# Optimization experiments

Hardware: AMD Instinct MI355X
Metric: run time of the kernel (lower is better)

Reference implementation:

```python
import jax, jax.numpy as jnp
import numpy as np

N_NODES = 10000
N_EDGES = 320000
HIDDEN = 64
IN_NODE = 4
IN_EDGE = 2
N_LAYERS = 4
COORDS_WEIGHT = 1.0
EPS = 1e-8


def _linear_params(key, fan_in, fan_out, scale=None, bias=True):
    k1, k2 = jax.random.split(key)
    s = scale if scale is not None else 1.0 / np.sqrt(fan_in)
    w = jax.random.uniform(k1, (fan_in, fan_out), jnp.float32, -s, s)
    b = jax.random.uniform(k2, (fan_out,), jnp.float32, -s, s) if bias else None
    return w, b


def setup_inputs() -> dict:
    key = jax.random.key(0)
    ks = jax.random.split(key, 16)
    his = jax.random.normal(ks[0], (N_NODES, IN_NODE), jnp.float32)
    loc = jax.random.normal(ks[1], (N_NODES, 3), jnp.float32)
    vel = jax.random.normal(ks[2], (N_NODES, 3), jnp.float32)
    edges = jax.random.randint(ks[3], (2, N_EDGES), 0, N_NODES, jnp.int64)
    edge_attr = jax.random.normal(ks[4], (N_EDGES, IN_EDGE), jnp.float32)
    emb_w, emb_b = _linear_params(ks[5], IN_NODE, HIDDEN)
    # edge MLP: cat(h_i, h_j, radial, edge_attr) -> hidden -> hidden
    edge_in = 2 * HIDDEN + 1 + IN_EDGE
    edge_w1, edge_b1 = _linear_params(ks[6], edge_in, HIDDEN)
    edge_w2, edge_b2 = _linear_params(ks[7], HIDDEN, HIDDEN)
    # node MLP: cat(h, agg) -> hidden -> hidden
    node_w1, node_b1 = _linear_params(ks[8], 2 * HIDDEN, HIDDEN)
    node_w2, node_b2 = _linear_params(ks[9], HIDDEN, HIDDEN)
    # coord MLP: hidden -> hidden -> 1 (last layer xavier-small, no bias, as in EGNN)
    coord_w1, coord_b1 = _linear_params(ks[10], HIDDEN, HIDDEN)
    coord_w2 = jax.random.normal(ks[11], (HIDDEN, 1), jnp.float32) * 0.001
    # coord_mlp_vel: hidden -> hidden -> 1
    vel_w1, vel_b1 = _linear_params(ks[12], HIDDEN, HIDDEN)
    vel_w2, vel_b2 = _linear_params(ks[13], HIDDEN, 1)
    return dict(his=his, loc=loc, edges=edges, vel=vel, edge_attr=edge_attr,
                emb_w=emb_w, emb_b=emb_b,
                edge_w1=edge_w1, edge_b1=edge_b1, edge_w2=edge_w2, edge_b2=edge_b2,
                node_w1=node_w1, node_b1=node_b1, node_w2=node_w2, node_b2=node_b2,
                coord_w1=coord_w1, coord_b1=coord_b1, coord_w2=coord_w2,
                vel_w1=vel_w1, vel_b1=vel_b1, vel_w2=vel_w2, vel_b2=vel_b2)


def _segment_mean(data, seg, num_segments):
    s = jax.ops.segment_sum(data, seg, num_segments=num_segments)
    cnt = jax.ops.segment_sum(jnp.ones((data.shape[0], 1), data.dtype), seg, num_segments=num_segments)
    return s / jnp.clip(cnt, 1.0, None)


def _egcl_vel(h, row, col, coord, vel, init_vel, edge_attr, p):
    """One E_GCL_ERGN_vel call: equivariant message passing + 2nd-order update."""
    n = h.shape[0]
    coord_diff = coord[row] - coord[col]                       # [E,3]
    radial = jnp.sum(coord_diff * coord_diff, axis=-1, keepdims=True)  # [E,1]
    # edge model
    e_in = jnp.concatenate([h[row], h[col], radial, edge_attr], axis=-1)
    ef = jax.nn.silu(e_in @ p['edge_w1'] + p['edge_b1'])
    ef = jax.nn.silu(ef @ p['edge_w2'] + p['edge_b2'])         # [E,H]
    # coord (acceleration) model
    gate = jax.nn.silu(ef @ p['coord_w1'] + p['coord_b1']) @ p['coord_w2']  # [E,1]
    acc = _segment_mean(coord_diff * gate, row, n) * COORDS_WEIGHT          # [N,3]
    # velocity model (norm_vel=True: normalize initial velocity direction)
    iv = init_vel / (jnp.linalg.norm(init_vel, axis=-1, keepdims=True) + EPS)
    phi = jax.nn.silu(h @ p['vel_w1'] + p['vel_b1']) @ p['vel_w2'] + p['vel_b2']  # [N,1]
    vel_new = vel + acc + phi * iv
    coord_new = coord + vel_new
    # node model
    agg = jax.ops.segment_sum(ef, row, num_segments=n)         # [N,H]
    hn = jax.nn.silu(jnp.concatenate([h, agg], axis=-1) @ p['node_w1'] + p['node_b1'])
    hn = hn @ p['node_w2'] + p['node_b2']                      # recurrent=False
    return hn, coord_new, vel_new


def reference(his, loc, edges, vel, edge_attr,
              emb_w, emb_b,
              edge_w1, edge_b1, edge_w2, edge_b2,
              node_w1, node_b1, node_w2, node_b2,
              coord_w1, coord_b1, coord_w2,
              vel_w1, vel_b1, vel_w2, vel_b2):
    p = dict(edge_w1=edge_w1, edge_b1=edge_b1, edge_w2=edge_w2, edge_b2=edge_b2,
             node_w1=node_w1, node_b1=node_b1, node_w2=node_w2, node_b2=node_b2,
             coord_w1=coord_w1, coord_b1=coord_b1, coord_w2=coord_w2,
             vel_w1=vel_w1, vel_b1=vel_b1, vel_w2=vel_w2, vel_b2=vel_b2)
    row, col = edges[0], edges[1]
    his_e = his @ emb_w + emb_b                                # embedding
    hi, x, v = _egcl_vel(his_e, row, col, loc, vel, vel, edge_attr, p)
    h = his_e + hi                                             # residual accumulation
    for _ in range(1, N_LAYERS):                               # shared layer, n_layers iters
        hi, x, v = _egcl_vel(h, row, col, x, v, vel, edge_attr, p)
        h = h + hi
    return x, h, v


if __name__ == '__main__':
    out = reference(**setup_inputs())
    print([o.shape for o in out])
```

## Files before the change

### kernel.cpp

```cpp
#include <hip/hip_runtime.h>
#include <math.h>

#define N_NODES 10000
#define N_EDGES 320000
#define HID 64
#define N_LAYERS 4
#define EDGE_BLOCKS 2500
#define EDGE_TILES_PER_WAVE 2
#define N_TILES_NODE 625
#define ALD 72

typedef unsigned short ushort_t;
typedef unsigned int uint_t;
typedef __attribute__((ext_vector_type(8))) short short8;
typedef __attribute__((ext_vector_type(4))) float floatx4;

__device__ __forceinline__ float silu_f(float x) {
    return x * (1.0f / (1.0f + __expf(-x)));
}
__device__ __forceinline__ ushort_t f2bf(float f) {
    uint_t u = __float_as_uint(f);
    uint_t r = u + 0x7FFFu + ((u >> 16) & 1u);
    return (ushort_t)(r >> 16);
}
__device__ __forceinline__ float bf2f(ushort_t u) {
    return __uint_as_float(((uint_t)u) << 16);
}

__global__ void init_kernel(const float* __restrict__ loc, const float* __restrict__ vel,
                            float* __restrict__ x, float* __restrict__ v, float* __restrict__ iv) {
    int i = blockIdx.x * blockDim.x + threadIdx.x;
    if (i >= N_NODES) return;
    float v0 = vel[3*i], v1 = vel[3*i+1], v2 = vel[3*i+2];
    float nrm = sqrtf(v0*v0 + v1*v1 + v2*v2) + 1e-8f;
    x[3*i] = loc[3*i]; x[3*i+1] = loc[3*i+1]; x[3*i+2] = loc[3*i+2];
    v[3*i] = v0; v[3*i+1] = v1; v[3*i+2] = v2;
    iv[3*i] = v0/nrm; iv[3*i+1] = v1/nrm; iv[3*i+2] = v2/nrm;
}

__global__ __launch_bounds__(64) void embed_kernel(const float* __restrict__ his,
                                                   const float* __restrict__ w,
                                                   const float* __restrict__ b,
                                                   float* __restrict__ h0,
                                                   ushort_t* __restrict__ hbf) {
    int i = blockIdx.x, l = threadIdx.x;
    float acc = b[l];
    #pragma unroll
    for (int k = 0; k < 4; ++k) acc += his[i*4+k] * w[k*HID+l];
    h0[i*HID+l] = acc;
    hbf[i*HID+l] = f2bf(acc);
}

__global__ void count_kernel(const int* __restrict__ erow, int* __restrict__ counts) {
    int e = blockIdx.x * blockDim.x + threadIdx.x;
    if (e < N_EDGES) atomicAdd(&counts[erow[e]], 1);
}

__global__ __launch_bounds__(256) void scan_kernel(const int* __restrict__ counts,
                                                   int* __restrict__ offs) {
    __shared__ int part[256];
    const int t = threadIdx.x;
    const int base = t * 40;
    int s0 = 0;
    for (int k = 0; k < 40; ++k) {
        int i = base + k;
        if (i < N_NODES) s0 += counts[i];
    }
    part[t] = s0;
    __syncthreads();
    for (int d = 1; d < 256; d <<= 1) {
        int vv = (t >= d) ? part[t-d] : 0;
        __syncthreads();
        part[t] += vv;
        __syncthreads();
    }
    int run = part[t] - s0;
    for (int k = 0; k < 40; ++k) {
        int i = base + k;
        if (i < N_NODES) { run += counts[i]; offs[i+1] = run; }
    }
    if (t == 0) offs[0] = 0;
}

__global__ void scatter_kernel(const int* __restrict__ erow, const int* __restrict__ ecol,
                               const float* __restrict__ eattr,
                               const int* __restrict__ offs,
                               int* __restrict__ cursor,
                               int* __restrict__ srow, int* __restrict__ scol,
                               float* __restrict__ seattr) {
    int e = blockIdx.x * blockDim.x + threadIdx.x;
    if (e < N_EDGES) {
        int r = erow[e];
        int p = atomicAdd(&cursor[r], 1);
        int pos = offs[r] + p;
        srow[pos] = r;
        scol[pos] = ecol[e];
        seattr[2*pos]   = eattr[2*e];
        seattr[2*pos+1] = eattr[2*e+1];
    }
}

__device__ __forceinline__ void pack_one(const float* __restrict__ src, ushort_t* __restrict__ dst,
                                         int u) {
    int kt = u >> 8, nt = (u >> 6) & 3, lane = u & 63;
    int quad = lane >> 4, lo = lane & 15;
    #pragma unroll
    for (int j = 0; j < 8; ++j) {
        int k = 32*kt + quad*8 + j, n = 16*nt + lo;
        dst[(size_t)u*8 + j] = f2bf(src[k*HID + n]);
    }
}
__global__ void pack_weights(const float* __restrict__ ew1, const float* __restrict__ ew2,
                             const float* __restrict__ cw1, const float* __restrict__ nw1,
                             const float* __restrict__ nw2, const float* __restrict__ vw1,
                             ushort_t* __restrict__ pw1, ushort_t* __restrict__ pw2,
                             ushort_t* __restrict__ pc1, ushort_t* __restrict__ pn1,
                             ushort_t* __restrict__ pn2, ushort_t* __restrict__ pv1) {
    int t = blockIdx.x * blockDim.x + threadIdx.x;
    if      (t < 1024) pack_one(ew1, pw1, t);
    else if (t < 1536) pack_one(ew2, pw2, t - 1024);
    else if (t < 2048) pack_one(cw1, pc1, t - 1536);
    else if (t < 3072) pack_one(nw1, pn1, t - 2048);
    else if (t < 3584) pack_one(nw2, pn2, t - 3072);
    else               pack_one(vw1, pv1, t - 3584);
}

__global__ __launch_bounds__(256) void edge_kernel(
    const ushort_t* __restrict__ hbf, const float* __restrict__ x,
    const int* __restrict__ srow, const int* __restrict__ scol,
    const float* __restrict__ seattr,
    const float* __restrict__ ew1,
    const float* __restrict__ eb1, const float* __restrict__ eb2,
    const float* __restrict__ cb1, const float* __restrict__ cw2,
    const ushort_t* __restrict__ pw1, const ushort_t* __restrict__ pw2,
    const ushort_t* __restrict__ pc1,
    float* __restrict__ aggf, float* __restrict__ accf)
{
    __shared__ ushort_t sW1[4*4*64*8];
    __shared__ ushort_t sW2[2*4*64*8];
    __shared__ ushort_t sC1[2*4*64*8];
    __shared__ float sRW[3][HID];
    __shared__ float sB1[HID], sB2[HID], sCB1[HID], sCW2[HID];
    __shared__ ushort_t sAct[4][16*ALD];
    __shared__ float sEdge[4][16][8];

    for (int i = threadIdx.x; i < 4*4*64*8; i += 256) sW1[i] = pw1[i];
    for (int i = threadIdx.x; i < 2*4*64*8; i += 256) { sW2[i] = pw2[i]; sC1[i] = pc1[i]; }
    for (int i = threadIdx.x; i < 3*HID; i += 256) sRW[i/HID][i%HID] = ew1[(128 + i/HID)*HID + (i%HID)];
    if (threadIdx.x < HID) {
        sB1[threadIdx.x]  = eb1[threadIdx.x];
        sB2[threadIdx.x]  = eb2[threadIdx.x];
        sCB1[threadIdx.x] = cb1[threadIdx.x];
        sCW2[threadIdx.x] = cw2[threadIdx.x];
    }
    __syncthreads();

    const int wave = threadIdx.x >> 6, lane = threadIdx.x & 63;
    const int quad = lane >> 4, lo = lane & 15;
    ushort_t* act = sAct[wave];
    float (*sed)[8] = sEdge[wave];

    int tile = blockIdx.x * 4 + wave;
    for (int it = 0; it < EDGE_TILES_PER_WAVE; ++it, tile += EDGE_BLOCKS*4) {
        const int p0 = tile * 16;
        const int rme = srow[p0 + lo], cme = scol[p0 + lo];
        if (lane < 16) {
            float d0 = x[3*rme]   - x[3*cme];
            float d1 = x[3*rme+1] - x[3*cme+1];
            float d2 = x[3*rme+2] - x[3*cme+2];
            sed[lane][0] = d0; sed[lane][1] = d1; sed[lane][2] = d2;
            sed[lane][3] = d0*d0 + d1*d1 + d2*d2;
            sed[lane][4] = seattr[2*(p0+lane)]; sed[lane][5] = seattr[2*(p0+lane)+1];
        }
        const ushort_t* hr = hbf + (size_t)rme * HID;
        const ushort_t* hc = hbf + (size_t)cme * HID;
        short8 af0 = *(const short8*)(hr + quad*8);
        short8 af1 = *(const short8*)(hr + 32 + quad*8);
        short8 af2 = *(const short8*)(hc + quad*8);
        short8 af3 = *(const short8*)(hc + 32 + quad*8);
        __syncthreads();

        floatx4 acc[4];
        #pragma unroll
        for (int nt = 0; nt < 4; ++nt) {
            floatx4 a = {0.f, 0.f, 0.f, 0.f};
            a = __builtin_amdgcn_mfma_f32_16x16x32_bf16(af0, *(const short8*)(sW1 + ((0*4+nt)*64+lane)*8), a, 0, 0, 0);
            a = __builtin_amdgcn_mfma_f32_16x16x32_bf16(af1, *(const short8*)(sW1 + ((1*4+nt)*64+lane)*8), a, 0, 0, 0);
            a = __builtin_amdgcn_mfma_f32_16x16x32_bf16(af2, *(const short8*)(sW1 + ((2*4+nt)*64+lane)*8), a, 0, 0, 0);
            a = __builtin_amdgcn_mfma_f32_16x16x32_bf16(af3, *(const short8*)(sW1 + ((3*4+nt)*64+lane)*8), a, 0, 0, 0);
            acc[nt] = a;
        }
        float rad[4], ea0[4], ea1[4];
        #pragma unroll
        for (int r = 0; r < 4; ++r) {
            const int m = 4*quad + r;
            rad[r] = sed[m][3]; ea0[r] = sed[m][4]; ea1[r] = sed[m][5];
        }
        #pragma unroll
        for (int nt = 0; nt < 4; ++nt) {
            const int n = 16*nt + lo;
            const float w128 = sRW[0][n], w129 = sRW[1][n], w130 = sRW[2][n], b1 = sB1[n];
            #pragma unroll
            for (int r = 0; r < 4; ++r) {
                float v = acc[nt][r] + rad[r]*w128 + ea0[r]*w129 + ea1[r]*w130 + b1;
                act[(4*quad + r)*ALD + n] = f2bf(silu_f(v));
            }
        }
        __syncthreads();

        short8 g0 = *(const short8*)(act + lo*ALD + quad*8);
        short8 g1 = *(const short8*)(act + lo*ALD + 32 + quad*8);
        floatx4 acc2[4];
        #pragma unroll
        for (int nt = 0; nt < 4; ++nt) {
            floatx4 a = {0.f, 0.f, 0.f, 0.f};
            a = __builtin_amdgcn_mfma_f32_16x16x32_bf16(g0, *(const short8*)(sW2 + ((0*4+nt)*64+lane)*8), a, 0, 0, 0);
            a = __builtin_amdgcn_mfma_f32_16x16x32_bf16(g1, *(const short8*)(sW2 + ((1*4+nt)*64+lane)*8), a, 0, 0, 0);
            acc2[nt] = a;
        }
        __syncthreads();
        #pragma unroll
        for (int nt = 0; nt < 4; ++nt) {
            const int n = 16*nt + lo;
            const float b2 = sB2[n];
            #pragma unroll
            for (int r = 0; r < 4; ++r)
                act[(4*quad + r)*ALD + n] = f2bf(silu_f(acc2[nt][r] + b2));
        }
        __syncthreads();

        {
            float s = 0.f;
            #pragma unroll
            for (int m = 0; m < 16; ++m) {
                s += bf2f(act[m*ALD + lane]);
                const int rm = __shfl(rme, m, 64);
                const int rn = (m < 15) ? __shfl(rme, m + 1, 64) : -1;
                if (rm != rn) {
                    atomicAdd(&aggf[(size_t)rm*HID + lane], s);
                    s = 0.f;
                }
            }
        }

        short8 q0 = *(const short8*)(act + lo*ALD + quad*8);
        short8 q1 = *(const short8*)(act + lo*ALD + 32 + quad*8);
        float gs[4] = {0.f, 0.f, 0.f, 0.f};
        #pragma unroll
        for (int nt = 0; nt < 4; ++nt) {
            floatx4 a = {0.f, 0.f, 0.f, 0.f};
            a = __builtin_amdgcn_mfma_f32_16x16x32_bf16(q0, *(const short8*)(sC1 + ((0*4+nt)*64+lane)*8), a, 0, 0, 0);
            a = __builtin_amdgcn_mfma_f32_16x16x32_bf16(q1, *(const short8*)(sC1 + ((1*4+nt)*64+lane)*8), a, 0, 0, 0);
            const int n = 16*nt + lo;
            const float cb = sCB1[n], cw = sCW2[n];
            #pragma unroll
            for (int r = 0; r < 4; ++r) gs[r] += silu_f(a[r] + cb) * cw;
        }
        #pragma unroll
        for (int off = 1; off < 16; off <<= 1) {
            #pragma unroll
            for (int r = 0; r < 4; ++r) gs[r] += __shfl_xor(gs[r], off, 64);
        }
        int rr[4];
        #pragma unroll
        for (int r = 0; r < 4; ++r) rr[r] = __shfl(rme, 4*quad + r, 64);
        if (lo < 3) {
            #pragma unroll
            for (int r = 0; r < 4; ++r) {
                const int m = 4*quad + r;
                atomicAdd(&accf[(size_t)rr[r]*3 + lo], sed[m][lo] * gs[r]);
            }
        }
        __syncthreads();
    }
}

__global__ __launch_bounds__(256) void node_kernel(
    const float* __restrict__ h_in, float* __restrict__ h_out, ushort_t* __restrict__ hbf,
    float* __restrict__ x, float* __restrict__ v, const float* __restrict__ iv,
    const float* __restrict__ aggf, const float* __restrict__ accf,
    const int* __restrict__ offs,
    const ushort_t* __restrict__ pn1, const ushort_t* __restrict__ pn2,
    const ushort_t* __restrict__ pv1,
    const float* __restrict__ nb1, const float* __restrict__ nb2,
    const float* __restrict__ vb1, const float* __restrict__ vb2,
    const float* __restrict__ vw2)
{
    __shared__ ushort_t sT1[4][16*ALD];
    __shared__ float sPhi[4][16];

    const int wave = threadIdx.x >> 6, lane = threadIdx.x & 63;
    const int tile = blockIdx.x * 4 + wave;
    if (tile >= N_TILES_NODE) return;
    const int quad = lane >> 4, lo = lane & 15;
    const int i0 = tile * 16;
    ushort_t* t1 = sT1[wave];

    int ov = 0;
    if (lane < 17) ov = offs[i0 + lane];

    const ushort_t* hrow = hbf + (size_t)(i0 + lo) * HID;
    short8 af0 = *(const short8*)(hrow + quad*8);
    short8 af1 = *(const short8*)(hrow + 32 + quad*8);
    const float* ag = aggf + (size_t)(i0 + lo) * HID + quad*8;
    short8 af2, af3;
    #pragma unroll
    for (int j = 0; j < 8; ++j) {
        af2[j] = (short)f2bf(ag[j]);
        af3[j] = (short)f2bf(ag[32 + j]);
    }

    #pragma unroll
    for (int nt = 0; nt < 4; ++nt) {
        floatx4 a = {0.f, 0.f, 0.f, 0.f};
        a = __builtin_amdgcn_mfma_f32_16x16x32_bf16(af0, *(const short8*)(pn1 + ((size_t)(0*4+nt)*64+lane)*8), a, 0, 0, 0);
        a = __builtin_amdgcn_mfma_f32_16x16x32_bf16(af1, *(const short8*)(pn1 + ((size_t)(1*4+nt)*64+lane)*8), a, 0, 0, 0);
        a = __builtin_amdgcn_mfma_f32_16x16x32_bf16(af2, *(const short8*)(pn1 + ((size_t)(2*4+nt)*64+lane)*8), a, 0, 0, 0);
        a = __builtin_amdgcn_mfma_f32_16x16x32_bf16(af3, *(const short8*)(pn1 + ((size_t)(3*4+nt)*64+lane)*8), a, 0, 0, 0);
        const int n = 16*nt + lo;
        const float b1 = nb1[n];
        #pragma unroll
        for (int r = 0; r < 4; ++r)
            t1[(4*quad + r)*ALD + n] = f2bf(silu_f(a[r] + b1));
    }

    short8 g0 = *(const short8*)(t1 + lo*ALD + quad*8);
    short8 g1 = *(const short8*)(t1 + lo*ALD + 32 + quad*8);
    #pragma unroll
    for (int nt = 0; nt < 4; ++nt) {
        floatx4 a = {0.f, 0.f, 0.f, 0.f};
        a = __builtin_amdgcn_mfma_f32_16x16x32_bf16(g0, *(const short8*)(pn2 + ((size_t)(0*4+nt)*64+lane)*8), a, 0, 0, 0);
        a = __builtin_amdgcn_mfma_f32_16x16x32_bf16(g1, *(const short8*)(pn2 + ((size_t)(1*4+nt)*64+lane)*8), a, 0, 0, 0);
        const int n = 16*nt + lo;
        const float b2 = nb2[n];
        #pragma unroll
        for (int r = 0; r < 4; ++r) {
            const int i = i0 + 4*quad + r;
            const float hnew = h_in[(size_t)i*HID + n] + a[r] + b2;
            h_out[(size_t)i*HID + n] = hnew;
            hbf[(size_t)i*HID + n] = f2bf(hnew);
        }
    }

    float gs[4] = {0.f, 0.f, 0.f, 0.f};
    #pragma unroll
    for (int nt = 0; nt < 4; ++nt) {
        floatx4 a = {0.f, 0.f, 0.f, 0.f};
        a = __builtin_amdgcn_mfma_f32_16x16x32_bf16(af0, *(const short8*)(pv1 + ((size_t)(0*4+nt)*64+lane)*8), a, 0, 0, 0);
        a = __builtin_amdgcn_mfma_f32_16x16x32_bf16(af1, *(const short8*)(pv1 + ((size_t)(1*4+nt)*64+lane)*8), a, 0, 0, 0);
        const int n = 16*nt + lo;
        const float b1 = vb1[n], w2 = vw2[n];
        #pragma unroll
        for (int r = 0; r < 4; ++r) gs[r] += silu_f(a[r] + b1) * w2;
    }
    #pragma unroll
    for (int off = 1; off < 16; off <<= 1) {
        #pragma unroll
        for (int r = 0; r < 4; ++r) gs[r] += __shfl_xor(gs[r], off, 64);
    }
    const float vb2s = vb2[0];
    if (lo == 0) {
        #pragma unroll
        for (int r = 0; r < 4; ++r) sPhi[wave][4*quad + r] = gs[r] + vb2s;
    }

    if (lane < 48) {
        const int m = lane / 3, d = lane - m*3;
        const int s = __shfl(ov, m, 64), t = __shfl(ov, m + 1, 64);
        const int cnt = t - s;
        const int i = i0 + m;
        const float accm = accf[(size_t)i*3 + d] / (float)(cnt > 0 ? cnt : 1);
        const float phi = sPhi[wave][m];
        const float vn = v[3*i + d] + accm + phi * iv[3*i + d];
        v[3*i + d] = vn;
        x[3*i + d] += vn;
    }
}

__global__ void out_kernel(const float* __restrict__ x, const float* __restrict__ h,
                           const float* __restrict__ v, float* __restrict__ out) {
    int j = blockIdx.x * blockDim.x + threadIdx.x;
    const int nx = 3*N_NODES, nh = HID*N_NODES;
    if (j >= nx + nh + nx) return;
    if (j < nx) out[j] = x[j];
    else if (j < nx + nh) out[j] = h[j - nx];
    else out[j] = v[j - nx - nh];
}

extern "C" void kernel_launch(void* const* d_in, const int* in_sizes, int n_in,
                              void* d_out, int out_size, void* d_ws, size_t ws_size,
                              hipStream_t stream) {
    const float* his   = (const float*)d_in[0];
    const float* loc   = (const float*)d_in[1];
    const int*   edges = (const int*)  d_in[2];
    const float* vel   = (const float*)d_in[3];
    const float* eattr = (const float*)d_in[4];
    const float* emb_w = (const float*)d_in[5];
    const float* emb_b = (const float*)d_in[6];
    const float* ew1 = (const float*)d_in[7];
    const float* eb1 = (const float*)d_in[8];
    const float* ew2 = (const float*)d_in[9];
    const float* eb2 = (const float*)d_in[10];
    const float* nw1 = (const float*)d_in[11];
    const float* nb1 = (const float*)d_in[12];
    const float* nw2 = (const float*)d_in[13];
    const float* nb2 = (const float*)d_in[14];
    const float* cw1 = (const float*)d_in[15];
    const float* cb1 = (const float*)d_in[16];
    const float* cw2 = (const float*)d_in[17];
    const float* vw1 = (const float*)d_in[18];
    const float* vb1 = (const float*)d_in[19];
    const float* vw2 = (const float*)d_in[20];
    const float* vb2 = (const float*)d_in[21];

    const int* erow = edges;
    const int* ecol = edges + N_EDGES;

    char* ws = (char*)d_ws;
    size_t off = 0;
    auto walloc = [&](size_t bytes) -> void* {
        void* p = ws + off; off += (bytes + 255) & ~(size_t)255; return p;
    };
    float* h_a      = (float*)walloc((size_t)N_NODES*HID*4);
    float* h_b      = (float*)walloc((size_t)N_NODES*HID*4);
    ushort_t* hbf   = (ushort_t*)walloc((size_t)N_NODES*HID*2);
    float* xb       = (float*)walloc((size_t)N_NODES*3*4);
    float* vb       = (float*)walloc((size_t)N_NODES*3*4);
    float* ivb      = (float*)walloc((size_t)N_NODES*3*4);
    float* aggf     = (float*)walloc((size_t)N_NODES*HID*4);
    float* accf     = (float*)walloc((size_t)N_NODES*3*4);
    int* counts     = (int*)walloc((size_t)N_NODES*4);
    int* cursor     = (int*)walloc((size_t)N_NODES*4);
    int* offs       = (int*)walloc((size_t)(N_NODES+1)*4);
    int* srow       = (int*)walloc((size_t)N_EDGES*4);
    int* scol       = (int*)walloc((size_t)N_EDGES*4);
    float* seattr   = (float*)walloc((size_t)N_EDGES*2*4);
    ushort_t* pw1   = (ushort_t*)walloc((size_t)4*4*64*8*2);
    ushort_t* pw2   = (ushort_t*)walloc((size_t)2*4*64*8*2);
    ushort_t* pc1   = (ushort_t*)walloc((size_t)2*4*64*8*2);
    ushort_t* pn1   = (ushort_t*)walloc((size_t)4*4*64*8*2);
    ushort_t* pn2   = (ushort_t*)walloc((size_t)2*4*64*8*2);
    ushort_t* pv1   = (ushort_t*)walloc((size_t)2*4*64*8*2);

    (void)hipMemsetAsync(counts, 0, (size_t)N_NODES*4, stream);
    (void)hipMemsetAsync(cursor, 0, (size_t)N_NODES*4, stream);

    init_kernel<<<(N_NODES+255)/256, 256, 0, stream>>>(loc, vel, xb, vb, ivb);
    embed_kernel<<<N_NODES, 64, 0, stream>>>(his, emb_w, emb_b, h_a, hbf);
    count_kernel<<<(N_EDGES+255)/256, 256, 0, stream>>>(erow, counts);
    scan_kernel<<<1, 256, 0, stream>>>(counts, offs);
    scatter_kernel<<<(N_EDGES+255)/256, 256, 0, stream>>>(erow, ecol, eattr, offs, cursor,
                                                          srow, scol, seattr);
    pack_weights<<<16, 256, 0, stream>>>(ew1, ew2, cw1, nw1, nw2, vw1,
                                         pw1, pw2, pc1, pn1, pn2, pv1);

    float* h_cur = h_a;
    float* h_nxt = h_b;
    for (int layer = 0; layer < N_LAYERS; ++layer) {
        (void)hipMemsetAsync(aggf, 0, (size_t)N_NODES*HID*4, stream);
        (void)hipMemsetAsync(accf, 0, (size_t)N_NODES*3*4, stream);
        edge_kernel<<<EDGE_BLOCKS, 256, 0, stream>>>(hbf, xb, srow, scol, seattr,
                                                     ew1, eb1, eb2, cb1, cw2,
                                                     pw1, pw2, pc1, aggf, accf);
        node_kernel<<<(N_TILES_NODE+3)/4, 256, 0, stream>>>(h_cur, h_nxt, hbf, xb, vb, ivb,
                                                            aggf, accf, offs,
                                                            pn1, pn2, pv1,
                                                            nb1, nb2, vb1, vb2, vw2);
        float* tmp = h_cur; h_cur = h_nxt; h_nxt = tmp;
    }
    const int total = 3*N_NODES + HID*N_NODES + 3*N_NODES;
    out_kernel<<<(total+255)/256, 256, 0, stream>>>(xb, h_cur, vb, (float*)d_out);
}
```

Before: 550.3 us.

## Drop block barriers, fuse aggregation atomics into epilogue, zero accumulators in node kernel

Removes every __syncthreads from the edge kernel loop, relying on each wave owning its own LDS tile. The edge-feature aggregation now issues atomics directly from the MFMA output layout, merging only within each lane's 4 rows instead of scanning all 16 rows through LDS. This skips a barrier and an LDS pass, but likely issues several times more global atomics because sorted rows form long runs. The per-layer memsets of the aggregation buffers are replaced by zeroing in the node kernel after reading, with a single memset before the loop.

Result: slower. 678.4 us (+23.3%).

```diff
diff --git a/kernel.cpp b/kernel.cpp
--- a/kernel.cpp
+++ b/kernel.cpp
@@ -172,13 +172,16 @@
             sed[lane][3] = d0*d0 + d1*d1 + d2*d2;
             sed[lane][4] = seattr[2*(p0+lane)]; sed[lane][5] = seattr[2*(p0+lane)+1];
         }
+        int rr[4];
+        #pragma unroll
+        for (int r = 0; r < 4; ++r) rr[r] = __shfl(rme, 4*quad + r, 64);
+
         const ushort_t* hr = hbf + (size_t)rme * HID;
         const ushort_t* hc = hbf + (size_t)cme * HID;
         short8 af0 = *(const short8*)(hr + quad*8);
         short8 af1 = *(const short8*)(hr + 32 + quad*8);
         short8 af2 = *(const short8*)(hc + quad*8);
         short8 af3 = *(const short8*)(hc + 32 + quad*8);
-        __syncthreads();
 
         floatx4 acc[4];
         #pragma unroll
@@ -206,7 +209,6 @@
                 act[(4*quad + r)*ALD + n] = f2bf(silu_f(v));
             }
         }
-        __syncthreads();
 
         short8 g0 = *(const short8*)(act + lo*ALD + quad*8);
         short8 g1 = *(const short8*)(act + lo*ALD + 32 + quad*8);
@@ -218,26 +220,18 @@
             a = __builtin_amdgcn_mfma_f32_16x16x32_bf16(g1, *(const short8*)(sW2 + ((1*4+nt)*64+lane)*8), a, 0, 0, 0);
             acc2[nt] = a;
         }
-        __syncthreads();
         #pragma unroll
         for (int nt = 0; nt < 4; ++nt) {
             const int n = 16*nt + lo;
             const float b2 = sB2[n];
-            #pragma unroll
-            for (int r = 0; r < 4; ++r)
-                act[(4*quad + r)*ALD + n] = f2bf(silu_f(acc2[nt][r] + b2));
-        }
-        __syncthreads();
-
-        {
             float s = 0.f;
             #pragma unroll
-            for (int m = 0; m < 16; ++m) {
-                s += bf2f(act[m*ALD + lane]);
-                const int rm = __shfl(rme, m, 64);
-                const int rn = (m < 15) ? __shfl(rme, m + 1, 64) : -1;
-                if (rm != rn) {
-                    atomicAdd(&aggf[(size_t)rm*HID + lane], s);
+            for (int r = 0; r < 4; ++r) {
+                const float efv = silu_f(acc2[nt][r] + b2);
+                act[(4*quad + r)*ALD + n] = f2bf(efv);
+                s += efv;
+                if (r == 3 || rr[r] != rr[r+1]) {
+                    atomicAdd(&aggf[(size_t)rr[r]*HID + n], s);
                     s = 0.f;
                 }
             }
@@ -261,9 +255,6 @@
             #pragma unroll
             for (int r = 0; r < 4; ++r) gs[r] += __shfl_xor(gs[r], off, 64);
         }
-        int rr[4];
-        #pragma unroll
-        for (int r = 0; r < 4; ++r) rr[r] = __shfl(rme, 4*quad + r, 64);
         if (lo < 3) {
             #pragma unroll
             for (int r = 0; r < 4; ++r) {
@@ -271,14 +262,13 @@
                 atomicAdd(&accf[(size_t)rr[r]*3 + lo], sed[m][lo] * gs[r]);
             }
         }
-        __syncthreads();
     }
 }
 
 __global__ __launch_bounds__(256) void node_kernel(
     const float* __restrict__ h_in, float* __restrict__ h_out, ushort_t* __restrict__ hbf,
     float* __restrict__ x, float* __restrict__ v, const float* __restrict__ iv,
-    const float* __restrict__ aggf, const float* __restrict__ accf,
+    float* __restrict__ aggf, float* __restrict__ accf,
     const int* __restrict__ offs,
     const ushort_t* __restrict__ pn1, const ushort_t* __restrict__ pn2,
     const ushort_t* __restrict__ pv1,
@@ -302,13 +292,18 @@
     const ushort_t* hrow = hbf + (size_t)(i0 + lo) * HID;
     short8 af0 = *(const short8*)(hrow + quad*8);
     short8 af1 = *(const short8*)(hrow + 32 + quad*8);
-    const float* ag = aggf + (size_t)(i0 + lo) * HID + quad*8;
+    float* ag = aggf + (size_t)(i0 + lo) * HID + quad*8;
     short8 af2, af3;
     #pragma unroll
     for (int j = 0; j < 8; ++j) {
         af2[j] = (short)f2bf(ag[j]);
         af3[j] = (short)f2bf(ag[32 + j]);
     }
+    floatx4 z = {0.f, 0.f, 0.f, 0.f};
+    *(floatx4*)(ag)        = z;
+    *(floatx4*)(ag + 4)    = z;
+    *(floatx4*)(ag + 32)   = z;
+    *(floatx4*)(ag + 36)   = z;
 
     #pragma unroll
     for (int nt = 0; nt < 4; ++nt) {
@@ -370,6 +365,7 @@
         const int cnt = t - s;
         const int i = i0 + m;
         const float accm = accf[(size_t)i*3 + d] / (float)(cnt > 0 ? cnt : 1);
+        accf[(size_t)i*3 + d] = 0.f;
         const float phi = sPhi[wave][m];
         const float vn = v[3*i + d] + accm + phi * iv[3*i + d];
         v[3*i + d] = vn;
@@ -444,6 +440,8 @@
 
     (void)hipMemsetAsync(counts, 0, (size_t)N_NODES*4, stream);
     (void)hipMemsetAsync(cursor, 0, (size_t)N_NODES*4, stream);
+    (void)hipMemsetAsync(aggf, 0, (size_t)N_NODES*HID*4, stream);
+    (void)hipMemsetAsync(accf, 0, (size_t)N_NODES*3*4, stream);
 
     init_kernel<<<(N_NODES+255)/256, 256, 0, stream>>>(loc, vel, xb, vb, ivb);
     embed_kernel<<<N_NODES, 64, 0, stream>>>(his, emb_w, emb_b, h_a, hbf);
@@ -457,8 +455,6 @@
     float* h_cur = h_a;
     float* h_nxt = h_b;
     for (int layer = 0; layer < N_LAYERS; ++layer) {
-        (void)hipMemsetAsync(aggf, 0, (size_t)N_NODES*HID*4, stream);
-        (void)hipMemsetAsync(accf, 0, (size_t)N_NODES*3*4, stream);
         edge_kernel<<<EDGE_BLOCKS, 256, 0, stream>>>(hbf, xb, srow, scol, seattr,
                                                      ew1, eb1, eb2, cb1, cw2,
                                                      pw1, pw2, pc1, aggf, accf);
```
